# Optimization experiments

Measured on AMD Instinct MI355X. Metric: run time of the kernel, lower is better.

The kernel has to match this reference:

```python
import jax, jax.numpy as jnp
import numpy as np

N = 100000
E_RAND = 800000
IN_D, HID_D, OUT_D = 128, 64, 64
PROP_STEP = 8
ATTN_AFT = PROP_STEP // 2  # attention applied after this many prop steps
LAM = 1.0
ALP = 1.0 / (LAM + 1.0)    # alp=0 in init -> DGL auto-sets 1/(lam+1)
TAU = 0.2
P_RHO = 1.0
T_UP = -1.0                # T<=0 -> no upper threshold


def setup_inputs() -> dict:
    key = jax.random.key(0)
    k1, k2, k3, k4, k5 = jax.random.split(key, 5)
    loops = jnp.arange(N)
    src = jnp.concatenate([jax.random.randint(k1, (E_RAND,), 0, N), loops]).astype(jnp.int32)
    dst = jnp.concatenate([jax.random.randint(k2, (E_RAND,), 0, N), loops]).astype(jnp.int32)
    feat = jax.random.normal(k3, (N, IN_D), jnp.float32)
    # xavier_normal init, zero bias (as in MLP.reset_params)
    W_bef = jax.random.normal(k4, (IN_D, HID_D), jnp.float32) * np.float32(np.sqrt(2.0 / (IN_D + HID_D)))
    b_bef = jnp.zeros((HID_D,), jnp.float32)
    W_aft = jax.random.normal(k5, (HID_D, OUT_D), jnp.float32) * np.float32(np.sqrt(2.0 / (HID_D + OUT_D)))
    b_aft = jnp.zeros((OUT_D,), jnp.float32)
    return {"feat": feat, "W_bef": W_bef, "b_bef": b_bef, "W_aft": W_aft, "b_aft": b_aft, "src": src, "dst": dst}


def _ax(src, dst, w, X):
    # Y = A X with per-edge weights: scatter-add of w_e * X[src_e] into dst_e
    return jax.ops.segment_sum(X[src] * w[:, None], dst, num_segments=N)


def _attention(src, dst, Y):
    hs, hd = Y[src], Y[dst]  # [E, d]
    w = jnp.sum(hs * hs, -1) + jnp.sum(hd * hd, -1) - 2.0 * jnp.sum(hs * hd, -1)  # ||h_u - h_v||^2
    w = jax.nn.relu(w) + 1e-7
    w = jnp.power(w, 1.0 - 0.5 * P_RHO)
    w = jnp.maximum(w, TAU)  # lower threshold tau (in-place clamp in torch)
    if T_UP > 0:
        w = jnp.where(w > T_UP, jnp.inf, w)
    w = 1.0 / w + 1e-9
    deg = jax.ops.segment_sum(w, dst, num_segments=N)  # copy_e -> sum per dst node
    return w, deg


def _prop(src, dst, w, deg, Y, X):
    dt = LAM * deg + (1.0 - LAM)
    nrm = jnp.power(dt, -0.5)[:, None]
    py = nrm * _ax(src, dst, w, nrm * Y)
    return (1.0 - ALP) * Y + ALP * LAM * py + ALP * (X / dt[:, None])


def reference(feat, W_bef, b_bef, W_aft, b_aft, src, dst):
    X = feat @ W_bef + b_bef  # mlp_bef: single Linear(input_d, hidden_d)
    w = jnp.ones(src.shape[0], feat.dtype)  # initial edge weights = 1
    deg = jax.ops.segment_sum(w, dst, num_segments=N)  # in-degrees
    Y = X
    for k in range(PROP_STEP):
        Y = _prop(src, dst, w, deg, Y, X)
        if k == ATTN_AFT - 1:
            w, deg = _attention(src, dst, Y)
    # mlp_aft: init_activate=True (relu; norm='none', dropout=0) then Linear(hidden_d, output_d)
    return jax.nn.relu(Y) @ W_aft + b_aft
```

## Files before the change

kernel.cpp:

```cpp
#include <hip/hip_runtime.h>
#include <math.h>

#define IN_D 128
#define HID 64

typedef unsigned short ushort_t;
typedef unsigned int uint_t;

static __device__ __forceinline__ ushort_t f2bf(float f) {
    uint_t x = __float_as_uint(f);
    uint_t r = x + 0x7fffu + ((x >> 16) & 1u);
    return (ushort_t)(r >> 16);
}
static __device__ __forceinline__ float bf2f(ushort_t u) {
    return __uint_as_float(((uint_t)u) << 16);
}


__global__ void zero2_kernel(int* a, int* b, int n) {
    int i = blockIdx.x * blockDim.x + threadIdx.x;
    if (i < n) { a[i] = 0; b[i] = 0; }
}

__global__ void hist_kernel(const int* __restrict__ dst, int E, int* __restrict__ cnt) {
    int e = blockIdx.x * blockDim.x + threadIdx.x;
    if (e < E) atomicAdd(&cnt[dst[e]], 1);
}

__global__ void scan1_kernel(const int* __restrict__ cnt, int N,
                             int* __restrict__ row_ptr, int* __restrict__ blocksum,
                             float* __restrict__ nrm, float* __restrict__ invdt) {
    __shared__ int sm[1024];
    int i = blockIdx.x * 1024 + threadIdx.x;
    int v = (i < N) ? cnt[i] : 0;
    if (i < N) {
        float d = (float)v;
        nrm[i] = 1.0f / sqrtf(d);
        invdt[i] = 1.0f / d;
    }
    sm[threadIdx.x] = v;
    __syncthreads();
    for (int off = 1; off < 1024; off <<= 1) {
        int t = (threadIdx.x >= off) ? sm[threadIdx.x - off] : 0;
        __syncthreads();
        sm[threadIdx.x] += t;
        __syncthreads();
    }
    if (i < N) row_ptr[i + 1] = sm[threadIdx.x];
    if (threadIdx.x == 1023) blocksum[blockIdx.x] = sm[1023];
}

__global__ void scan2_kernel(int* __restrict__ blocksum, int nb) {
    __shared__ int sm[1024];
    int v = (threadIdx.x < nb) ? blocksum[threadIdx.x] : 0;
    sm[threadIdx.x] = v;
    __syncthreads();
    for (int off = 1; off < 1024; off <<= 1) {
        int t = (threadIdx.x >= off) ? sm[threadIdx.x - off] : 0;
        __syncthreads();
        sm[threadIdx.x] += t;
        __syncthreads();
    }
    if (threadIdx.x < nb) blocksum[threadIdx.x] = sm[threadIdx.x] - v;
}

__global__ void scan3_kernel(int* __restrict__ row_ptr, int N, const int* __restrict__ blocksum) {
    int i = blockIdx.x * 1024 + threadIdx.x;
    if (i < N) row_ptr[i + 1] += blocksum[blockIdx.x];
    if (i == 0) row_ptr[0] = 0;
}

__global__ void scatter_kernel(const int* __restrict__ src, const int* __restrict__ dst, int E,
                               const int* __restrict__ row_ptr, int* __restrict__ cursor,
                               const float* __restrict__ nrm,
                               int* __restrict__ src_perm, float* __restrict__ coef) {
    int e = blockIdx.x * blockDim.x + threadIdx.x;
    if (e < E) {
        int d = dst[e];
        int s = src[e];
        int pos = row_ptr[d] + atomicAdd(&cursor[d], 1);
        src_perm[pos] = s;
        coef[pos] = nrm[s];
    }
}

__global__ void nrm_from_deg(const float* __restrict__ deg, int N,
                             float* __restrict__ nrm, float* __restrict__ invdt) {
    int i = blockIdx.x * blockDim.x + threadIdx.x;
    if (i < N) {
        float dt = deg[i];
        nrm[i] = 1.0f / sqrtf(dt);
        invdt[i] = 1.0f / dt;
    }
}

__global__ void coef_kernel(const int* __restrict__ src_perm, const float* __restrict__ w_perm,
                            const float* __restrict__ nrm, int E, float* __restrict__ coef) {
    int e = blockIdx.x * blockDim.x + threadIdx.x;
    if (e < E) coef[e] = w_perm[e] * nrm[src_perm[e]];
}


__global__ __launch_bounds__(256) void prop_kernel(
    const float* __restrict__ Yin, const ushort_t* __restrict__ Ybf,
    const float* __restrict__ X,
    const int* __restrict__ row_ptr, const int* __restrict__ src_perm,
    const float* __restrict__ coef, const float* __restrict__ nrm,
    const float* __restrict__ invdt, int N,
    float* __restrict__ Yout, ushort_t* __restrict__ Yout_bf) {
    int wave = (blockIdx.x * blockDim.x + threadIdx.x) >> 6;
    int lane = threadIdx.x & 63;
    if (wave >= N) return;
    int r0 = row_ptr[wave], r1 = row_ptr[wave + 1];
    float acc = 0.0f;
    for (int jb = r0; jb < r1; jb += 64) {
        int m = r1 - jb;
        if (m > 64) m = 64;
        int sv = 0;
        float cv = 0.0f;
        if (lane < m) { sv = src_perm[jb + lane]; cv = coef[jb + lane]; }
        for (int t = 0; t < m; t += 8) {
            float v[8], c[8];
            #pragma unroll
            for (int u = 0; u < 8; ++u) {
                int idx = t + u;
                int active = idx < m;
                if (!active) idx = 0;
                int s = __shfl(sv, idx, 64);
                float cc = __shfl(cv, idx, 64);
                c[u] = active ? cc : 0.0f;
                v[u] = bf2f(Ybf[(size_t)s * HID + lane]);
            }
            #pragma unroll
            for (int u = 0; u < 8; ++u) acc += c[u] * v[u];
        }
    }
    size_t base = (size_t)wave * HID + lane;
    float out = 0.5f * Yin[base] + (0.5f * nrm[wave]) * acc + (0.5f * invdt[wave]) * X[base];
    Yout[base] = out;
    Yout_bf[base] = f2bf(out);
}

__global__ __launch_bounds__(256) void attn_kernel(
    const float* __restrict__ Y, const ushort_t* __restrict__ Ybf,
    const int* __restrict__ row_ptr, const int* __restrict__ src_perm, int N,
    float* __restrict__ w_perm, float* __restrict__ deg) {
    int wv = (blockIdx.x * blockDim.x + threadIdx.x) >> 6;
    int lane = threadIdx.x & 63;
    if (wv >= N) return;
    int r0 = row_ptr[wv], r1 = row_ptr[wv + 1];
    float hd = Y[(size_t)wv * HID + lane];
    float dacc = 0.0f;
    for (int jb = r0; jb < r1; jb += 64) {
        int m = r1 - jb;
        if (m > 64) m = 64;
        int sv = (lane < m) ? src_perm[jb + lane] : 0;
        float wreg = 0.0f;
        for (int t = 0; t < m; t += 8) {
            float ss[8];
            int act[8];
            #pragma unroll
            for (int u = 0; u < 8; ++u) {
                int idx = t + u;
                act[u] = idx < m;
                if (!act[u]) idx = 0;
                int s = __shfl(sv, idx, 64);
                float d = bf2f(Ybf[(size_t)s * HID + lane]) - hd;
                ss[u] = d * d;
            }
            #pragma unroll
            for (int o = 32; o >= 1; o >>= 1) {
                #pragma unroll
                for (int u = 0; u < 8; ++u) ss[u] += __shfl_xor(ss[u], o, 64);
            }
            #pragma unroll
            for (int u = 0; u < 8; ++u) {
                float w = fmaxf(ss[u], 0.0f) + 1e-7f;
                w = sqrtf(w);
                w = fmaxf(w, 0.2f);
                w = 1.0f / w + 1e-9f;
                if (act[u]) {
                    dacc += w;
                    if (lane == t + u) wreg = w;
                }
            }
        }
        if (lane < m) w_perm[jb + lane] = wreg;
    }
    if (lane == 0) deg[wv] = dacc;
}

__global__ __launch_bounds__(256) void gemm1_kernel(
    const float* __restrict__ feat, const float* __restrict__ W,
    const float* __restrict__ b, int N, float* __restrict__ X, ushort_t* __restrict__ Xbf) {
    __shared__ float Wl[IN_D * HID];
    __shared__ float featL[8 * IN_D];
    for (int i = threadIdx.x; i < IN_D * HID; i += 256) Wl[i] = W[i];
    int c = threadIdx.x & 63;
    int rsub = threadIdx.x >> 6;
    float bias = b[c];
    int ngroups = N / 8;
    const float4* feat4 = (const float4*)feat;
    for (int g = blockIdx.x; g < ngroups; g += gridDim.x) {
        __syncthreads();
        ((float4*)featL)[threadIdx.x] = feat4[(size_t)g * 256 + threadIdx.x];
        __syncthreads();
        const float4* f0 = (const float4*)&featL[rsub * IN_D];
        const float4* f1 = (const float4*)&featL[(rsub + 4) * IN_D];
        float acc0 = bias, acc1 = bias;
        #pragma unroll
        for (int k4 = 0; k4 < IN_D / 4; ++k4) {
            float4 a = f0[k4];
            float4 e = f1[k4];
            float w0 = Wl[(4 * k4 + 0) * HID + c];
            float w1 = Wl[(4 * k4 + 1) * HID + c];
            float w2 = Wl[(4 * k4 + 2) * HID + c];
            float w3 = Wl[(4 * k4 + 3) * HID + c];
            acc0 += a.x * w0 + a.y * w1 + a.z * w2 + a.w * w3;
            acc1 += e.x * w0 + e.y * w1 + e.z * w2 + e.w * w3;
        }
        size_t row = (size_t)g * 8;
        X[(row + rsub) * HID + c] = acc0;
        X[(row + rsub + 4) * HID + c] = acc1;
        Xbf[(row + rsub) * HID + c] = f2bf(acc0);
        Xbf[(row + rsub + 4) * HID + c] = f2bf(acc1);
    }
}

__global__ __launch_bounds__(256) void gemm2_kernel(
    const float* __restrict__ Y, const float* __restrict__ W,
    const float* __restrict__ b, int N, float* __restrict__ out) {
    __shared__ float Wl[HID * HID];
    __shared__ float Yl[8 * HID];
    for (int i = threadIdx.x; i < HID * HID; i += 256) Wl[i] = W[i];
    int c = threadIdx.x & 63;
    int rsub = threadIdx.x >> 6;
    float bias = b[c];
    int ngroups = N / 8;
    const float4* Y4 = (const float4*)Y;
    for (int g = blockIdx.x; g < ngroups; g += gridDim.x) {
        __syncthreads();
        if (threadIdx.x < 128) {
            float4 v = Y4[(size_t)g * 128 + threadIdx.x];
            v.x = fmaxf(v.x, 0.0f); v.y = fmaxf(v.y, 0.0f);
            v.z = fmaxf(v.z, 0.0f); v.w = fmaxf(v.w, 0.0f);
            ((float4*)Yl)[threadIdx.x] = v;
        }
        __syncthreads();
        const float4* f0 = (const float4*)&Yl[rsub * HID];
        const float4* f1 = (const float4*)&Yl[(rsub + 4) * HID];
        float acc0 = bias, acc1 = bias;
        #pragma unroll
        for (int k4 = 0; k4 < HID / 4; ++k4) {
            float4 a = f0[k4];
            float4 e = f1[k4];
            float w0 = Wl[(4 * k4 + 0) * HID + c];
            float w1 = Wl[(4 * k4 + 1) * HID + c];
            float w2 = Wl[(4 * k4 + 2) * HID + c];
            float w3 = Wl[(4 * k4 + 3) * HID + c];
            acc0 += a.x * w0 + a.y * w1 + a.z * w2 + a.w * w3;
            acc1 += e.x * w0 + e.y * w1 + e.z * w2 + e.w * w3;
        }
        size_t row = (size_t)g * 8;
        out[(row + rsub) * HID + c] = acc0;
        out[(row + rsub + 4) * HID + c] = acc1;
    }
}


extern "C" void kernel_launch(void* const* d_in, const int* in_sizes, int n_in,
                              void* d_out, int out_size, void* d_ws, size_t ws_size,
                              hipStream_t stream) {
    const float* feat  = (const float*)d_in[0];
    const float* W_bef = (const float*)d_in[1];
    const float* b_bef = (const float*)d_in[2];
    const float* W_aft = (const float*)d_in[3];
    const float* b_aft = (const float*)d_in[4];
    const int*   src   = (const int*)d_in[5];
    const int*   dst   = (const int*)d_in[6];

    const int N = in_sizes[0] / IN_D;
    const int E = in_sizes[5];

    char* p = (char*)d_ws;
    auto alloc = [&](size_t bytes) -> void* {
        void* r = (void*)p;
        p += (bytes + 255) & ~(size_t)255;
        return r;
    };
    float*    X       = (float*)alloc((size_t)N * HID * 4);
    float*    Ya      = (float*)alloc((size_t)N * HID * 4);
    float*    Yb      = (float*)alloc((size_t)N * HID * 4);
    ushort_t* Xbf     = (ushort_t*)alloc((size_t)N * HID * 2);
    ushort_t* Yabf    = (ushort_t*)alloc((size_t)N * HID * 2);
    ushort_t* Ybbf    = (ushort_t*)alloc((size_t)N * HID * 2);
    int*      cnt     = (int*)alloc((size_t)N * 4);
    int*      cursor  = (int*)alloc((size_t)N * 4);
    int*      row_ptr = (int*)alloc((size_t)(N + 1) * 4);
    int*      blocksum= (int*)alloc(4096);
    int*      src_perm= (int*)alloc((size_t)E * 4);
    float*    w_perm  = (float*)alloc((size_t)E * 4);
    float*    coef    = (float*)alloc((size_t)E * 4);
    float*    deg     = (float*)alloc((size_t)N * 4);
    float*    nrm     = (float*)alloc((size_t)N * 4);
    float*    invdt   = (float*)alloc((size_t)N * 4);

    const int TB = 256;
    dim3 blk(TB);
    int gN   = (N + TB - 1) / TB;
    int gE   = (E + TB - 1) / TB;
    int gNW  = (N * 64 + TB - 1) / TB;
    int nb   = (N + 1023) / 1024;

    zero2_kernel<<<gN, blk, 0, stream>>>(cnt, cursor, N);
    hist_kernel<<<gE, blk, 0, stream>>>(dst, E, cnt);
    scan1_kernel<<<nb, 1024, 0, stream>>>(cnt, N, row_ptr, blocksum, nrm, invdt);
    scan2_kernel<<<1, 1024, 0, stream>>>(blocksum, nb);
    scan3_kernel<<<nb, 1024, 0, stream>>>(row_ptr, N, blocksum);
    scatter_kernel<<<gE, blk, 0, stream>>>(src, dst, E, row_ptr, cursor, nrm, src_perm, coef);

    gemm1_kernel<<<2048, blk, 0, stream>>>(feat, W_bef, b_bef, N, X, Xbf);

    prop_kernel<<<gNW, blk, 0, stream>>>(X,  Xbf,  X, row_ptr, src_perm, coef, nrm, invdt, N, Ya, Yabf);
    prop_kernel<<<gNW, blk, 0, stream>>>(Ya, Yabf, X, row_ptr, src_perm, coef, nrm, invdt, N, Yb, Ybbf);
    prop_kernel<<<gNW, blk, 0, stream>>>(Yb, Ybbf, X, row_ptr, src_perm, coef, nrm, invdt, N, Ya, Yabf);
    prop_kernel<<<gNW, blk, 0, stream>>>(Ya, Yabf, X, row_ptr, src_perm, coef, nrm, invdt, N, Yb, Ybbf);

    attn_kernel<<<gNW, blk, 0, stream>>>(Yb, Ybbf, row_ptr, src_perm, N, w_perm, deg);
    nrm_from_deg<<<gN, blk, 0, stream>>>(deg, N, nrm, invdt);
    coef_kernel<<<gE, blk, 0, stream>>>(src_perm, w_perm, nrm, E, coef);

    prop_kernel<<<gNW, blk, 0, stream>>>(Yb, Ybbf, X, row_ptr, src_perm, coef, nrm, invdt, N, Ya, Yabf);
    prop_kernel<<<gNW, blk, 0, stream>>>(Ya, Yabf, X, row_ptr, src_perm, coef, nrm, invdt, N, Yb, Ybbf);
    prop_kernel<<<gNW, blk, 0, stream>>>(Yb, Ybbf, X, row_ptr, src_perm, coef, nrm, invdt, N, Ya, Yabf);
    prop_kernel<<<gNW, blk, 0, stream>>>(Ya, Yabf, X, row_ptr, src_perm, coef, nrm, invdt, N, Yb, Ybbf);

    gemm2_kernel<<<512, blk, 0, stream>>>(Yb, W_aft, b_aft, N, (float*)d_out);
}
```

Measured before the change: 719.5 us.

## Restructure attention to thread-per-edge with separate degree reduction; unroll prop gather

```diff
diff --git a/kernel.cpp b/kernel.cpp
--- a/kernel.cpp
+++ b/kernel.cpp
@@ -17,9 +17,9 @@
 }
 
 
-__global__ void zero2_kernel(int* a, int* b, int n) {
+__global__ void zero1_kernel(int* a, int n) {
     int i = blockIdx.x * blockDim.x + threadIdx.x;
-    if (i < n) { a[i] = 0; b[i] = 0; }
+    if (i < n) a[i] = 0;
 }
 
 __global__ void hist_kernel(const int* __restrict__ dst, int E, int* __restrict__ cnt) {
@@ -27,13 +27,14 @@
     if (e < E) atomicAdd(&cnt[dst[e]], 1);
 }
 
-__global__ void scan1_kernel(const int* __restrict__ cnt, int N,
+__global__ void scan1_kernel(int* __restrict__ cnt, int N,
                              int* __restrict__ row_ptr, int* __restrict__ blocksum,
                              float* __restrict__ nrm, float* __restrict__ invdt) {
     __shared__ int sm[1024];
     int i = blockIdx.x * 1024 + threadIdx.x;
     int v = (i < N) ? cnt[i] : 0;
     if (i < N) {
+        cnt[i] = 0;
         float d = (float)v;
         nrm[i] = 1.0f / sqrtf(d);
         invdt[i] = 1.0f / d;
@@ -73,24 +74,16 @@
 __global__ void scatter_kernel(const int* __restrict__ src, const int* __restrict__ dst, int E,
                                const int* __restrict__ row_ptr, int* __restrict__ cursor,
                                const float* __restrict__ nrm,
-                               int* __restrict__ src_perm, float* __restrict__ coef) {
+                               int* __restrict__ src_perm, int* __restrict__ dst_perm,
+                               float* __restrict__ coef) {
     int e = blockIdx.x * blockDim.x + threadIdx.x;
     if (e < E) {
         int d = dst[e];
         int s = src[e];
         int pos = row_ptr[d] + atomicAdd(&cursor[d], 1);
         src_perm[pos] = s;
+        dst_perm[pos] = d;
         coef[pos] = nrm[s];
-    }
-}
-
-__global__ void nrm_from_deg(const float* __restrict__ deg, int N,
-                             float* __restrict__ nrm, float* __restrict__ invdt) {
-    int i = blockIdx.x * blockDim.x + threadIdx.x;
-    if (i < N) {
-        float dt = deg[i];
-        nrm[i] = 1.0f / sqrtf(dt);
-        invdt[i] = 1.0f / dt;
     }
 }
 
@@ -119,10 +112,10 @@
         int sv = 0;
         float cv = 0.0f;
         if (lane < m) { sv = src_perm[jb + lane]; cv = coef[jb + lane]; }
-        for (int t = 0; t < m; t += 8) {
-            float v[8], c[8];
+        for (int t = 0; t < m; t += 16) {
+            float v[16], c[16];
             #pragma unroll
-            for (int u = 0; u < 8; ++u) {
+            for (int u = 0; u < 16; ++u) {
                 int idx = t + u;
                 int active = idx < m;
                 if (!active) idx = 0;
@@ -132,7 +125,7 @@
                 v[u] = bf2f(Ybf[(size_t)s * HID + lane]);
             }
             #pragma unroll
-            for (int u = 0; u < 8; ++u) acc += c[u] * v[u];
+            for (int u = 0; u < 16; ++u) acc = fmaf(c[u], v[u], acc);
         }
     }
     size_t base = (size_t)wave * HID + lane;
@@ -141,53 +134,59 @@
     Yout_bf[base] = f2bf(out);
 }
 
-__global__ __launch_bounds__(256) void attn_kernel(
-    const float* __restrict__ Y, const ushort_t* __restrict__ Ybf,
-    const int* __restrict__ row_ptr, const int* __restrict__ src_perm, int N,
-    float* __restrict__ w_perm, float* __restrict__ deg) {
-    int wv = (blockIdx.x * blockDim.x + threadIdx.x) >> 6;
+__global__ __launch_bounds__(256) void attn_edge_kernel(
+    const ushort_t* __restrict__ Ybf,
+    const int* __restrict__ src_perm, const int* __restrict__ dst_perm,
+    int E, float* __restrict__ w_perm) {
+    int e = blockIdx.x * blockDim.x + threadIdx.x;
+    if (e >= E) return;
+    int s = src_perm[e], d = dst_perm[e];
+    const uint4* ps = (const uint4*)(Ybf + (size_t)s * HID);
+    const uint4* pd = (const uint4*)(Ybf + (size_t)d * HID);
+    uint4 a[8], b[8];
+    #pragma unroll
+    for (int i = 0; i < 8; ++i) a[i] = ps[i];
+    #pragma unroll
+    for (int i = 0; i < 8; ++i) b[i] = pd[i];
+    float ss = 0.0f;
+    #pragma unroll
+    for (int i = 0; i < 8; ++i) {
+        const uint_t* ua = (const uint_t*)&a[i];
+        const uint_t* ub = (const uint_t*)&b[i];
+        #pragma unroll
+        for (int j = 0; j < 4; ++j) {
+            float slo = __uint_as_float(ua[j] << 16);
+            float dlo = __uint_as_float(ub[j] << 16);
+            float shi = __uint_as_float(ua[j] & 0xffff0000u);
+            float dhi = __uint_as_float(ub[j] & 0xffff0000u);
+            float t0 = slo - dlo;
+            float t1 = shi - dhi;
+            ss = fmaf(t0, t0, ss);
+            ss = fmaf(t1, t1, ss);
+        }
+    }
+    float w = fmaxf(ss, 0.0f) + 1e-7f;
+    w = sqrtf(w);
+    w = fmaxf(w, 0.2f);
+    w = 1.0f / w + 1e-9f;
+    w_perm[e] = w;
+}
+
+__global__ __launch_bounds__(256) void deg_sum_kernel(
+    const float* __restrict__ w_perm, const int* __restrict__ row_ptr, int N,
+    float* __restrict__ nrm, float* __restrict__ invdt) {
+    int v = (blockIdx.x * blockDim.x + threadIdx.x) >> 6;
     int lane = threadIdx.x & 63;
-    if (wv >= N) return;
-    int r0 = row_ptr[wv], r1 = row_ptr[wv + 1];
-    float hd = Y[(size_t)wv * HID + lane];
-    float dacc = 0.0f;
-    for (int jb = r0; jb < r1; jb += 64) {
-        int m = r1 - jb;
-        if (m > 64) m = 64;
-        int sv = (lane < m) ? src_perm[jb + lane] : 0;
-        float wreg = 0.0f;
-        for (int t = 0; t < m; t += 8) {
-            float ss[8];
-            int act[8];
-            #pragma unroll
-            for (int u = 0; u < 8; ++u) {
-                int idx = t + u;
-                act[u] = idx < m;
-                if (!act[u]) idx = 0;
-                int s = __shfl(sv, idx, 64);
-                float d = bf2f(Ybf[(size_t)s * HID + lane]) - hd;
-                ss[u] = d * d;
-            }
-            #pragma unroll
-            for (int o = 32; o >= 1; o >>= 1) {
-                #pragma unroll
-                for (int u = 0; u < 8; ++u) ss[u] += __shfl_xor(ss[u], o, 64);
-            }
-            #pragma unroll
-            for (int u = 0; u < 8; ++u) {
-                float w = fmaxf(ss[u], 0.0f) + 1e-7f;
-                w = sqrtf(w);
-                w = fmaxf(w, 0.2f);
-                w = 1.0f / w + 1e-9f;
-                if (act[u]) {
-                    dacc += w;
-                    if (lane == t + u) wreg = w;
-                }
-            }
-        }
-        if (lane < m) w_perm[jb + lane] = wreg;
-    }
-    if (lane == 0) deg[wv] = dacc;
+    if (v >= N) return;
+    int r0 = row_ptr[v], r1 = row_ptr[v + 1];
+    float s = 0.0f;
+    for (int j = r0 + lane; j < r1; j += 64) s += w_perm[j];
+    #pragma unroll
+    for (int o = 32; o >= 1; o >>= 1) s += __shfl_xor(s, o, 64);
+    if (lane == 0) {
+        nrm[v] = 1.0f / sqrtf(s);
+        invdt[v] = 1.0f / s;
+    }
 }
 
 __global__ __launch_bounds__(256) void gemm1_kernel(
@@ -295,13 +294,12 @@
     ushort_t* Yabf    = (ushort_t*)alloc((size_t)N * HID * 2);
     ushort_t* Ybbf    = (ushort_t*)alloc((size_t)N * HID * 2);
     int*      cnt     = (int*)alloc((size_t)N * 4);
-    int*      cursor  = (int*)alloc((size_t)N * 4);
     int*      row_ptr = (int*)alloc((size_t)(N + 1) * 4);
     int*      blocksum= (int*)alloc(4096);
     int*      src_perm= (int*)alloc((size_t)E * 4);
+    int*      dst_perm= (int*)alloc((size_t)E * 4);
     float*    w_perm  = (float*)alloc((size_t)E * 4);
     float*    coef    = (float*)alloc((size_t)E * 4);
-    float*    deg     = (float*)alloc((size_t)N * 4);
     float*    nrm     = (float*)alloc((size_t)N * 4);
     float*    invdt   = (float*)alloc((size_t)N * 4);
 
@@ -312,12 +310,13 @@
     int gNW  = (N * 64 + TB - 1) / TB;
     int nb   = (N + 1023) / 1024;
 
-    zero2_kernel<<<gN, blk, 0, stream>>>(cnt, cursor, N);
+    zero1_kernel<<<gN, blk, 0, stream>>>(cnt, N);
     hist_kernel<<<gE, blk, 0, stream>>>(dst, E, cnt);
     scan1_kernel<<<nb, 1024, 0, stream>>>(cnt, N, row_ptr, blocksum, nrm, invdt);
     scan2_kernel<<<1, 1024, 0, stream>>>(blocksum, nb);
     scan3_kernel<<<nb, 1024, 0, stream>>>(row_ptr, N, blocksum);
-    scatter_kernel<<<gE, blk, 0, stream>>>(src, dst, E, row_ptr, cursor, nrm, src_perm, coef);
+    scatter_kernel<<<gE, blk, 0, stream>>>(src, dst, E, row_ptr, cnt, nrm,
+                                           src_perm, dst_perm, coef);
 
     gemm1_kernel<<<2048, blk, 0, stream>>>(feat, W_bef, b_bef, N, X, Xbf);
 
@@ -326,8 +325,8 @@
     prop_kernel<<<gNW, blk, 0, stream>>>(Yb, Ybbf, X, row_ptr, src_perm, coef, nrm, invdt, N, Ya, Yabf);
     prop_kernel<<<gNW, blk, 0, stream>>>(Ya, Yabf, X, row_ptr, src_perm, coef, nrm, invdt, N, Yb, Ybbf);
 
-    attn_kernel<<<gNW, blk, 0, stream>>>(Yb, Ybbf, row_ptr, src_perm, N, w_perm, deg);
-    nrm_from_deg<<<gN, blk, 0, stream>>>(deg, N, nrm, invdt);
+    attn_edge_kernel<<<gE, blk, 0, stream>>>(Ybbf, src_perm, dst_perm, E, w_perm);
+    deg_sum_kernel<<<gNW, blk, 0, stream>>>(w_perm, row_ptr, N, nrm, invdt);
     coef_kernel<<<gE, blk, 0, stream>>>(src_perm, w_perm, nrm, E, coef);
 
     prop_kernel<<<gNW, blk, 0, stream>>>(Yb, Ybbf, X, row_ptr, src_perm, coef, nrm, invdt, N, Ya, Yabf);
```

After: 641.1 us. -10.9%, faster.
